# Optimization experiments

Hardware: AMD Instinct MI355X
Metric: run time of the kernel (lower is better)

Reference implementation:

```python
import jax, jax.numpy as jnp
import numpy as np

# dims: S samples, J u-functions, D outputs, P input dims, N data points
S, J, D, P, N = 8, 4, 4, 3, 1024
BG, BU, MG, MU = 32, 32, 10, 32  # g-RFF, u-RFF, g-inducing, u-inducing


def setup_inputs() -> dict:
    key = jax.random.key(0)
    ks = jax.random.split(key, 16)
    ts = jax.random.normal(ks[0], (N, P), dtype=jnp.float32)
    alphas = jax.random.uniform(ks[1], (D, P), minval=0.5, maxval=1.5)   # filter window precisions
    pgs = jax.random.uniform(ks[2], (D, P), minval=0.5, maxval=1.5)      # g kernel precisions (ls2pr)
    zgs = jnp.tile(jnp.linspace(-1.0, 1.0, MG, dtype=jnp.float32)[:, None], (1, P))  # g inducing inputs
    thetag = 2.0 * jax.random.normal(ks[3], (D, P, BG))                  # g spectral freqs
    betag = jax.random.uniform(ks[4], (S, D, P, BG), minval=0.0, maxval=2 * np.pi)
    wg = jax.random.normal(ks[5], (S, D, P, BG)) / np.sqrt(BG)           # g RFF weights
    qg = 0.1 * jax.random.normal(ks[6], (S, D, P, MG))                   # g canonical weights (compute_q)
    pus = jax.random.uniform(ks[7], (P,), minval=0.5, maxval=1.5)        # u cross-kernel precisions
    zus = jax.random.normal(ks[8], (MU, P))                              # u inducing inputs
    thetau = 2.0 * jax.random.normal(ks[9], (S, J, P, BU))               # u spectral freqs
    betau = jax.random.uniform(ks[10], (S, J, BU), minval=0.0, maxval=2 * np.pi)
    wu = jax.random.normal(ks[11], (S, J, BU)) / np.sqrt(BU)
    qu = 0.1 * jax.random.normal(ks[12], (S, J, MU))                     # u canonical weights
    ampu = jnp.float32(1.0)
    log_amps = 0.1 * jax.random.normal(ks[13], (D, J))
    W = jax.random.normal(ks[14], (P, D)) / np.sqrt(P)
    return dict(ts=ts, alphas=alphas, pgs=pgs, zgs=zgs, thetag=thetag, betag=betag,
                wg=wg, qg=qg, pus=pus, zus=zus, thetau=thetau, betau=betau,
                wu=wu, qu=qu, ampu=ampu, log_amps=log_amps, W=W)


def reference(ts, alphas, pgs, zgs, thetag, betag, wg, qg, pus, zus,
              thetau, betau, wu, qu, ampu, log_amps, W):
    """NPGPLayer.forward: f_d(t) = sum_j amps[d,j] * I_dj(t) + ts @ W, where
    I_dj(t) = ampu * int_{R^P} [prod_p exp(-alpha_dp tau_p^2) g_dp(tau_p)] u_j(t - tau) dtau,
    with g, u sampled via random-Fourier + canonical (inducing) features; all 1-D
    Gaussian x cosine integrals are closed-form (this is the math of integrals.full_I)."""
    pi = jnp.pi
    amps = jnp.exp(log_amps)  # [D,J]

    # ---------- Part A: u RFF terms.  Fourier transform of windowed g at om ----------
    om = thetau  # [S,J,P,BU]
    aE = alphas[None, None, :, :, None, None]            # [1,1,D,P,1,1]
    th = thetag[None, None, :, :, None, :]               # [1,1,D,P,1,BG]
    omE = om[:, :, None, :, :, None]                     # [S,J,1,P,BU,1]
    e1 = jnp.exp(-(th - omE) ** 2 / (4 * aE))
    e2 = jnp.exp(-(th + omE) ** 2 / (4 * aE))
    cb = jnp.cos(betag)[:, None, :, :, None, :]
    sb = jnp.sin(betag)[:, None, :, :, None, :]
    wgE = wg[:, None, :, :, None, :]
    # int exp(-a tau^2) cos(th tau + b) e^{-i om tau} dtau
    Ghat_rff = jnp.sum(0.5 * jnp.sqrt(pi / aE) * wgE * ((e1 + e2) * cb + 1j * (e1 - e2) * sb), axis=-1)  # [S,J,D,P,BU]

    A = alphas + pgs                                     # [D,P]
    zT = zgs.T                                           # [P,MG]
    mu = pgs[:, :, None] * zT[None] / A[:, :, None]      # [D,P,MG]
    rg = alphas[:, :, None] * pgs[:, :, None] * zT[None] ** 2 / A[:, :, None]
    decay = jnp.exp(-om[:, :, None, :, :] ** 2 / (4 * A[None, None, :, :, None]))        # [S,J,D,P,BU]
    phase_mu = jnp.exp(-1j * om[:, :, None, :, :, None] * mu[None, None, :, :, None, :])  # [S,J,D,P,BU,MG]
    can_coef = jnp.sqrt(pi / A)[..., None] * jnp.exp(-rg)                                 # [D,P,MG]
    Ghat_can = jnp.sum(qg[:, None, :, :, None, :] * can_coef[None, None, :, :, None, :] * phase_mu, axis=-1) * decay
    Ghat = Ghat_rff + Ghat_can                           # [S,J,D,P,BU] complex

    phase_t = jnp.exp(1j * om[..., None] * ts.T[None, None, :, None, :])  # [S,J,P,BU,N]
    combined = Ghat[..., None] * phase_t[:, :, None]     # [S,J,D,P,BU,N]
    prodp = jnp.prod(combined, axis=3)                   # [S,J,D,BU,N]  (product over input dims)
    cu = wu * jnp.exp(1j * betau)                        # [S,J,BU]
    F_rff = jnp.real(jnp.einsum('sjb,sjdbn->sjdn', cu, prodp))

    # ---------- Part B: u canonical (inducing) terms -- Gaussian x Gaussian integrals ----------
    c = jnp.transpose(ts[:, None, :] - zus[None, :, :], (2, 0, 1))  # [P,N,MU]
    Bm = alphas + pus[None, :]                           # [D,P]
    mp = pus[None, :, None, None] * c[None] / Bm[:, :, None, None]                 # [D,P,N,MU]
    rp = alphas[:, :, None, None] * pus[None, :, None, None] * c[None] ** 2 / Bm[:, :, None, None]
    spec = jnp.sqrt(pi / Bm)[:, :, None] * jnp.exp(-thetag ** 2 / (4 * Bm[:, :, None]))  # [D,P,BG]
    arg = thetag[:, :, None, None, :] * mp[..., None]    # [D,P,N,MU,BG]
    cosx, sinx = jnp.cos(arg), jnp.sin(arg)
    coef1 = wg * jnp.cos(betag) * spec[None]             # [S,D,P,BG]
    coef2 = wg * jnp.sin(betag) * spec[None]
    term_rff = (jnp.einsum('dpnmb,sdpb->sdpnm', cosx, coef1)
                - jnp.einsum('dpnmb,sdpb->sdpnm', sinx, coef2)) * jnp.exp(-rp)[None]
    Cm = Bm + pgs                                        # [D,P]
    diff = mp[..., None] - zT[None, :, None, None, :]    # [D,P,N,MU,MG]
    r2 = Bm[:, :, None, None, None] * pgs[:, :, None, None, None] * diff ** 2 / Cm[:, :, None, None, None]
    val = jnp.sqrt(pi / Cm)[:, :, None, None, None] * jnp.exp(-rp[..., None] - r2)
    term_can = jnp.einsum('dpnmg,sdpg->sdpnm', val, qg)
    Gg = term_rff + term_can                             # [S,D,P,N,MU]
    prodg = jnp.prod(Gg, axis=2)                         # [S,D,N,MU]
    F_can = jnp.einsum('sjm,sdnm->sjdn', qu, prodg)

    F = ampu * (F_rff + F_can)                           # [S,J,D,N]
    layer = jnp.einsum('dj,sjdn->snd', amps, F)          # amps-weighted sum over u functions
    return layer + ts @ W                                # residual connection (is_final_layer=False)
```

## Files before the change

kernel.cpp:

```cpp
#include <hip/hip_runtime.h>
#include <math.h>

#define S_ 8
#define J_ 4
#define D_ 4
#define P_ 3
#define N_ 1024
#define BG_ 32
#define BU_ 32
#define MG_ 10
#define MU_ 32

static constexpr float PI_F = 3.14159265358979323846f;

#define COEF_OFF    0
#define CANPART_OFF 8192

#define NB_COEF 64
#define NB_CAN  512

__global__ __launch_bounds__(256, 4) void fused_kernel(
    const float* __restrict__ ts,     const float* __restrict__ alphas,
    const float* __restrict__ pgs,    const float* __restrict__ zgs,
    const float* __restrict__ thetag, const float* __restrict__ betag,
    const float* __restrict__ wg,     const float* __restrict__ qg,
    const float* __restrict__ pus,    const float* __restrict__ zus,
    const float* __restrict__ thetau, const float* __restrict__ betau,
    const float* __restrict__ wu,     const float* __restrict__ qu,
    const float* __restrict__ ampu_p, const float* __restrict__ log_amps,
    float* __restrict__ ws)
{
    int bid = blockIdx.x;
    int t   = threadIdx.x;
    float ampu = ampu_p[0];

    if (bid >= NB_COEF) {
        __shared__ float sc1[P_][BG_][S_];
        __shared__ float sc2[P_][BG_][S_];
        __shared__ float sqg[P_][MG_][S_];
        __shared__ float stg[P_][BG_];
        __shared__ float szg[P_][MG_];
        __shared__ float szu[P_][MU_];
        __shared__ float sts[8][P_];
        __shared__ float squ[S_][MU_];
        __shared__ float skmp[P_], skrp[P_], sksc[P_], skbc[P_];

        int cb = bid - NB_COEF;
        int d  = cb >> 7;
        int n0 = (cb & 127) * 8;

        for (int i = t; i < P_*BG_*S_; i += 256) {
            int p = i >> 8, b = (i >> 3) & 31, s = i & 7;
            float alpha = alphas[d*P_ + p];
            float Bm = alpha + pus[p];
            float th = thetag[(d*P_ + p)*BG_ + b];
            float spec = sqrtf(PI_F / Bm) * __expf(-th*th*0.25f/Bm);
            float be = betag[((s*D_ + d)*P_ + p)*BG_ + b];
            float w  = wg   [((s*D_ + d)*P_ + p)*BG_ + b];
            float sb, cbv; __sincosf(be, &sb, &cbv);
            sc1[p][b][s] = w * cbv * spec;
            sc2[p][b][s] = w * sb * spec;
        }
        for (int i = t; i < P_*MG_*S_; i += 256) {
            int p = i / (MG_*S_), r = i % (MG_*S_), g = r >> 3, s = r & 7;
            ((float*)sqg)[i] = qg[((s*D_ + d)*P_ + p)*MG_ + g];
        }
        {
            int s = t >> 5, m = t & 31;
            float acc = 0.f;
            #pragma unroll
            for (int j = 0; j < J_; ++j)
                acc += __expf(log_amps[d*J_ + j]) * qu[(s*J_ + j)*MU_ + m];
            squ[s][m] = ampu * acc;
        }
        if (t < P_*BG_) ((float*)stg)[t] = thetag[d*P_*BG_ + t];
        if (t < P_*MG_) { int p = t / MG_, g = t % MG_; szg[p][g] = zgs[g*P_ + p]; }
        if (t >= 128 && t < 128 + P_*MU_) {
            int i = t - 128; int p = i >> 5, m = i & 31;
            szu[p][m] = zus[m*P_ + p];
        }
        if (t >= 96 && t < 96 + 8*P_) { int i = t - 96; sts[i/3][i%3] = ts[n0*P_ + i]; }
        if (t >= 120 && t < 120 + P_) {
            int p = t - 120;
            float alpha = alphas[d*P_ + p], pg = pgs[d*P_ + p], pu = pus[p];
            float Bm = alpha + pu, invB = 1.f / Bm;
            skmp[p] = pu * invB;
            skrp[p] = alpha * pu * invB;
            float Cm = Bm + pg, invC = 1.f / Cm;
            sksc[p] = sqrtf(PI_F * invC);
            skbc[p] = Bm * pg * invC;
        }
        __syncthreads();

        int m = t & 31, q = (t >> 5) & 1, nl = t >> 6;
        int rA = nl*2, rB = nl*2 + 1;

        float pA0=1.f,pA1=1.f,pA2=1.f,pA3=1.f,pA4=1.f,pA5=1.f,pA6=1.f,pA7=1.f;
        float pB0=1.f,pB1=1.f,pB2=1.f,pB3=1.f,pB4=1.f,pB5=1.f,pB6=1.f,pB7=1.f;

        #pragma unroll 1
        for (int p = 0; p < P_; ++p) {
            float zu = szu[p][m];
            float cA = sts[rA][p] - zu;
            float cB = sts[rB][p] - zu;
            float mpA = skmp[p] * cA, mpB = skmp[p] * cB;
            float EA = __expf(-skrp[p] * cA * cA);
            float EB = __expf(-skrp[p] * cB * cB);

            float aA0=0.f,aA1=0.f,aA2=0.f,aA3=0.f,aA4=0.f,aA5=0.f,aA6=0.f,aA7=0.f;
            float aB0=0.f,aB1=0.f,aB2=0.f,aB3=0.f,aB4=0.f,aB5=0.f,aB6=0.f,aB7=0.f;

            int b0 = q * 16;
            #pragma unroll 2
            for (int bb = 0; bb < 16; ++bb) {
                int b = b0 + bb;
                float th = stg[p][b];
                float sxA, cxA; __sincosf(th * mpA, &sxA, &cxA);
                float sxB, cxB; __sincosf(th * mpB, &sxB, &cxB);
                const float4* c1v = (const float4*)&sc1[p][b][0];
                const float4* c2v = (const float4*)&sc2[p][b][0];
                float4 u0 = c1v[0], u1 = c1v[1];
                float4 v0 = c2v[0], v1 = c2v[1];
                aA0 += u0.x*cxA - v0.x*sxA;  aA1 += u0.y*cxA - v0.y*sxA;
                aA2 += u0.z*cxA - v0.z*sxA;  aA3 += u0.w*cxA - v0.w*sxA;
                aA4 += u1.x*cxA - v1.x*sxA;  aA5 += u1.y*cxA - v1.y*sxA;
                aA6 += u1.z*cxA - v1.z*sxA;  aA7 += u1.w*cxA - v1.w*sxA;
                aB0 += u0.x*cxB - v0.x*sxB;  aB1 += u0.y*cxB - v0.y*sxB;
                aB2 += u0.z*cxB - v0.z*sxB;  aB3 += u0.w*cxB - v0.w*sxB;
                aB4 += u1.x*cxB - v1.x*sxB;  aB5 += u1.y*cxB - v1.y*sxB;
                aB6 += u1.z*cxB - v1.z*sxB;  aB7 += u1.w*cxB - v1.w*sxB;
            }
            int g0 = q * 5;
            #pragma unroll 1
            for (int gg = 0; gg < 5; ++gg) {
                int g = g0 + gg;
                float zg = szg[p][g];
                float dA = mpA - zg, dB = mpB - zg;
                float vA = sksc[p] * __expf(-skbc[p]*dA*dA);
                float vB = sksc[p] * __expf(-skbc[p]*dB*dB);
                const float4* qv = (const float4*)&sqg[p][g][0];
                float4 q0 = qv[0], q1 = qv[1];
                aA0 += q0.x*vA; aA1 += q0.y*vA; aA2 += q0.z*vA; aA3 += q0.w*vA;
                aA4 += q1.x*vA; aA5 += q1.y*vA; aA6 += q1.z*vA; aA7 += q1.w*vA;
                aB0 += q0.x*vB; aB1 += q0.y*vB; aB2 += q0.z*vB; aB3 += q0.w*vB;
                aB4 += q1.x*vB; aB5 += q1.y*vB; aB6 += q1.z*vB; aB7 += q1.w*vB;
            }
            aA0 += __shfl_xor(aA0, 32, 64); aA1 += __shfl_xor(aA1, 32, 64);
            aA2 += __shfl_xor(aA2, 32, 64); aA3 += __shfl_xor(aA3, 32, 64);
            aA4 += __shfl_xor(aA4, 32, 64); aA5 += __shfl_xor(aA5, 32, 64);
            aA6 += __shfl_xor(aA6, 32, 64); aA7 += __shfl_xor(aA7, 32, 64);
            aB0 += __shfl_xor(aB0, 32, 64); aB1 += __shfl_xor(aB1, 32, 64);
            aB2 += __shfl_xor(aB2, 32, 64); aB3 += __shfl_xor(aB3, 32, 64);
            aB4 += __shfl_xor(aB4, 32, 64); aB5 += __shfl_xor(aB5, 32, 64);
            aB6 += __shfl_xor(aB6, 32, 64); aB7 += __shfl_xor(aB7, 32, 64);
            pA0 *= EA*aA0; pA1 *= EA*aA1; pA2 *= EA*aA2; pA3 *= EA*aA3;
            pA4 *= EA*aA4; pA5 *= EA*aA5; pA6 *= EA*aA6; pA7 *= EA*aA7;
            pB0 *= EB*aB0; pB1 *= EB*aB1; pB2 *= EB*aB2; pB3 *= EB*aB3;
            pB4 *= EB*aB4; pB5 *= EB*aB5; pB6 *= EB*aB6; pB7 *= EB*aB7;
        }

        float prodA[S_] = {pA0,pA1,pA2,pA3,pA4,pA5,pA6,pA7};
        float prodB[S_] = {pB0,pB1,pB2,pB3,pB4,pB5,pB6,pB7};
        int nA = n0 + rA, nB = n0 + rB;
        int s0 = q * 4;
        #pragma unroll
        for (int ss = 0; ss < 4; ++ss) {
            int s = ss + s0;
            float qu_sm = squ[s][m];
            float vA = qu_sm * prodA[s];
            float vB = qu_sm * prodB[s];
            #pragma unroll
            for (int off = 16; off; off >>= 1) {
                vA += __shfl_xor(vA, off, 32);
                vB += __shfl_xor(vB, off, 32);
            }
            if (m == 0) {
                ws[CANPART_OFF + (s*N_ + nA)*D_ + d] = vA;
                ws[CANPART_OFF + (s*N_ + nB)*D_ + d] = vB;
            }
        }
    } else {
        int gtid = bid * 256 + t;
        int q  = gtid & 3;
        int bu = (gtid >> 2) & 31;
        int d  = (gtid >> 7) & 3;
        int j  = (gtid >> 9) & 3;
        int s  = gtid >> 11;
        float G3r = 1.f, G3i = 0.f;
        #pragma unroll 1
        for (int p = 0; p < P_; ++p) {
            float alpha = alphas[d*P_ + p], pg = pgs[d*P_ + p];
            float om    = thetau[((s*J_ + j)*P_ + p)*BU_ + bu];
            float inv4a = 0.25f / alpha;
            float pref  = 0.5f * sqrtf(PI_F / alpha);
            float gr = 0.f, gi = 0.f;
            int b0 = q * 8;
            #pragma unroll 2
            for (int bb = 0; bb < 8; ++bb) {
                int b = b0 + bb;
                float th = thetag[(d*P_ + p)*BG_ + b];
                float dm = th - om, dpl = th + om;
                float e1 = __expf(-dm*dm*inv4a);
                float e2 = __expf(-dpl*dpl*inv4a);
                float be = betag[((s*D_ + d)*P_ + p)*BG_ + b];
                float w  = wg   [((s*D_ + d)*P_ + p)*BG_ + b];
                float sb, cb; __sincosf(be, &sb, &cb);
                gr += pref * w * (e1 + e2) * cb;
                gi += pref * w * (e1 - e2) * sb;
            }
            float A = alpha + pg, invA = 1.f / A;
            float decay = __expf(-om*om*0.25f*invA);
            float cc    = sqrtf(PI_F * invA);
            float cr = 0.f, ci = 0.f;
            int g0 = q * 3, gn = (q < 3) ? 3 : 1;
            #pragma unroll 1
            for (int gg = 0; gg < gn; ++gg) {
                int g = g0 + gg;
                float z  = zgs[g*P_ + p];
                float mu = pg * z * invA;
                float rg = alpha * pg * z * z * invA;
                float cg = cc * __expf(-rg);
                float qv = qg[((s*D_ + d)*P_ + p)*MG_ + g];
                float sm, cm; __sincosf(om * mu, &sm, &cm);
                cr += qv * cg * cm;
                ci -= qv * cg * sm;
            }
            #pragma unroll
            for (int off = 1; off < 4; off <<= 1) {
                gr += __shfl_xor(gr, off, 4);
                gi += __shfl_xor(gi, off, 4);
                cr += __shfl_xor(cr, off, 4);
                ci += __shfl_xor(ci, off, 4);
            }
            float Gr = gr + decay * cr;
            float Gi = gi + decay * ci;
            float nr = G3r*Gr - G3i*Gi;
            float ni = G3r*Gi + G3i*Gr;
            G3r = nr; G3i = ni;
        }
        if (q == 0) {
            float bv = betau[(s*J_ + j)*BU_ + bu];
            float wv = wu   [(s*J_ + j)*BU_ + bu];
            float sbu, cbu; __sincosf(bv, &sbu, &cbu);
            float cuR = wv * cbu, cuI = wv * sbu;
            float amp = ampu * __expf(log_amps[d*J_ + j]);
            int base = (((s*J_ + j)*BU_ + bu)*D_ + d) * 2;
            ws[COEF_OFF + base    ] = amp * (cuR*G3r - cuI*G3i);
            ws[COEF_OFF + base + 1] = amp * (cuR*G3i + cuI*G3r);
        }
    }
}

__global__ __launch_bounds__(256, 4) void final_kernel(
    const float* __restrict__ ts, const float* __restrict__ thetau,
    const float* __restrict__ W,  const float* __restrict__ ws,
    float* __restrict__ out)
{
    __shared__ float sth[J_][P_][BU_];
    __shared__ float scf[J_*BU_][8];
    __shared__ float sW[P_][D_];

    int bid = blockIdx.x;
    int s  = bid >> 7;
    int n0 = (bid & 127) * 8;
    int t  = threadIdx.x;

    for (int i = t; i < J_*P_*BU_; i += 256) ((float*)sth)[i] = thetau[s*J_*P_*BU_ + i];
    for (int i = t; i < J_*BU_*8; i += 256)  ((float*)scf)[i] = ws[COEF_OFF + s*J_*BU_*8 + i];
    if (t < P_*D_) ((float*)sW)[t] = W[t];
    __syncthreads();

    int k = t & 31, nl = t >> 5;
    int n = n0 + nl;
    float t0 = ts[n*P_], t1 = ts[n*P_ + 1], t2 = ts[n*P_ + 2];

    float r0=0.f, r1=0.f, r2=0.f, r3=0.f;
    #pragma unroll 2
    for (int j = 0; j < J_; ++j) {
        float phi = sth[j][0][k]*t0 + sth[j][1][k]*t1 + sth[j][2][k]*t2;
        float sp, cp; __sincosf(phi, &sp, &cp);
        const float4* cfv = (const float4*)&scf[j*BU_ + k][0];
        float4 u = cfv[0], v = cfv[1];
        r0 += u.x*cp - u.y*sp;
        r1 += u.z*cp - u.w*sp;
        r2 += v.x*cp - v.y*sp;
        r3 += v.z*cp - v.w*sp;
    }
    #pragma unroll
    for (int off = 16; off; off >>= 1) {
        r0 += __shfl_xor(r0, off, 32);
        r1 += __shfl_xor(r1, off, 32);
        r2 += __shfl_xor(r2, off, 32);
        r3 += __shfl_xor(r3, off, 32);
    }
    if (k == 0) {
        const float4 cpart = *(const float4*)(ws + CANPART_OFF + (s*N_ + n)*D_);
        float4 o;
        o.x = cpart.x + r0 + t0*sW[0][0] + t1*sW[1][0] + t2*sW[2][0];
        o.y = cpart.y + r1 + t0*sW[0][1] + t1*sW[1][1] + t2*sW[2][1];
        o.z = cpart.z + r2 + t0*sW[0][2] + t1*sW[1][2] + t2*sW[2][2];
        o.w = cpart.w + r3 + t0*sW[0][3] + t1*sW[1][3] + t2*sW[2][3];
        *(float4*)(out + (s*N_ + n)*D_) = o;
    }
}

extern "C" void kernel_launch(void* const* d_in, const int* in_sizes, int n_in,
                              void* d_out, int out_size, void* d_ws, size_t ws_size,
                              hipStream_t stream)
{
    const float* ts       = (const float*)d_in[0];
    const float* alphas   = (const float*)d_in[1];
    const float* pgs      = (const float*)d_in[2];
    const float* zgs      = (const float*)d_in[3];
    const float* thetag   = (const float*)d_in[4];
    const float* betag    = (const float*)d_in[5];
    const float* wg       = (const float*)d_in[6];
    const float* qg       = (const float*)d_in[7];
    const float* pus      = (const float*)d_in[8];
    const float* zus      = (const float*)d_in[9];
    const float* thetau   = (const float*)d_in[10];
    const float* betau    = (const float*)d_in[11];
    const float* wu       = (const float*)d_in[12];
    const float* qu       = (const float*)d_in[13];
    const float* ampu     = (const float*)d_in[14];
    const float* log_amps = (const float*)d_in[15];
    const float* W        = (const float*)d_in[16];
    float* ws  = (float*)d_ws;
    float* out = (float*)d_out;

    fused_kernel<<<NB_COEF + NB_CAN, 256, 0, stream>>>(
        ts, alphas, pgs, zgs, thetag, betag, wg, qg,
        pus, zus, thetau, betau, wu, qu, ampu, log_amps, ws);
    final_kernel<<<1024, 256, 0, stream>>>(ts, thetau, W, ws, out);
}
```

Measured before the change: 26.04 us.

## Fold coefficient computation into every canonical block with per-warp coefficient slices

```diff
diff --git a/kernel.cpp b/kernel.cpp
--- a/kernel.cpp
+++ b/kernel.cpp
@@ -16,7 +16,6 @@
 #define COEF_OFF    0
 #define CANPART_OFF 8192
 
-#define NB_COEF 64
 #define NB_CAN  512
 
 __global__ __launch_bounds__(256, 4) void fused_kernel(
@@ -30,223 +29,214 @@
     const float* __restrict__ ampu_p, const float* __restrict__ log_amps,
     float* __restrict__ ws)
 {
+    __shared__ float sc1[P_][BG_][S_];
+    __shared__ float sc2[P_][BG_][S_];
+    __shared__ float sqg[P_][MG_][S_];
+    __shared__ float stg[P_][BG_];
+    __shared__ float szg[P_][MG_];
+    __shared__ float szu[P_][MU_];
+    __shared__ float sts[8][P_];
+    __shared__ float squ[S_][MU_];
+    __shared__ float skmp[P_], skrp[P_], sksc[P_], skbc[P_];
+
     int bid = blockIdx.x;
     int t   = threadIdx.x;
     float ampu = ampu_p[0];
 
-    if (bid >= NB_COEF) {
-        __shared__ float sc1[P_][BG_][S_];
-        __shared__ float sc2[P_][BG_][S_];
-        __shared__ float sqg[P_][MG_][S_];
-        __shared__ float stg[P_][BG_];
-        __shared__ float szg[P_][MG_];
-        __shared__ float szu[P_][MU_];
-        __shared__ float sts[8][P_];
-        __shared__ float squ[S_][MU_];
-        __shared__ float skmp[P_], skrp[P_], sksc[P_], skbc[P_];
-
-        int cb = bid - NB_COEF;
-        int d  = cb >> 7;
-        int n0 = (cb & 127) * 8;
-
-        for (int i = t; i < P_*BG_*S_; i += 256) {
-            int p = i >> 8, b = (i >> 3) & 31, s = i & 7;
-            float alpha = alphas[d*P_ + p];
-            float Bm = alpha + pus[p];
-            float th = thetag[(d*P_ + p)*BG_ + b];
-            float spec = sqrtf(PI_F / Bm) * __expf(-th*th*0.25f/Bm);
-            float be = betag[((s*D_ + d)*P_ + p)*BG_ + b];
-            float w  = wg   [((s*D_ + d)*P_ + p)*BG_ + b];
-            float sb, cbv; __sincosf(be, &sb, &cbv);
-            sc1[p][b][s] = w * cbv * spec;
-            sc2[p][b][s] = w * sb * spec;
-        }
-        for (int i = t; i < P_*MG_*S_; i += 256) {
-            int p = i / (MG_*S_), r = i % (MG_*S_), g = r >> 3, s = r & 7;
-            ((float*)sqg)[i] = qg[((s*D_ + d)*P_ + p)*MG_ + g];
-        }
-        {
-            int s = t >> 5, m = t & 31;
-            float acc = 0.f;
-            #pragma unroll
-            for (int j = 0; j < J_; ++j)
-                acc += __expf(log_amps[d*J_ + j]) * qu[(s*J_ + j)*MU_ + m];
-            squ[s][m] = ampu * acc;
-        }
-        if (t < P_*BG_) ((float*)stg)[t] = thetag[d*P_*BG_ + t];
-        if (t < P_*MG_) { int p = t / MG_, g = t % MG_; szg[p][g] = zgs[g*P_ + p]; }
-        if (t >= 128 && t < 128 + P_*MU_) {
-            int i = t - 128; int p = i >> 5, m = i & 31;
-            szu[p][m] = zus[m*P_ + p];
-        }
-        if (t >= 96 && t < 96 + 8*P_) { int i = t - 96; sts[i/3][i%3] = ts[n0*P_ + i]; }
-        if (t >= 120 && t < 120 + P_) {
-            int p = t - 120;
-            float alpha = alphas[d*P_ + p], pg = pgs[d*P_ + p], pu = pus[p];
-            float Bm = alpha + pu, invB = 1.f / Bm;
-            skmp[p] = pu * invB;
-            skrp[p] = alpha * pu * invB;
-            float Cm = Bm + pg, invC = 1.f / Cm;
-            sksc[p] = sqrtf(PI_F * invC);
-            skbc[p] = Bm * pg * invC;
-        }
-        __syncthreads();
-
-        int m = t & 31, q = (t >> 5) & 1, nl = t >> 6;
-        int rA = nl*2, rB = nl*2 + 1;
-
-        float pA0=1.f,pA1=1.f,pA2=1.f,pA3=1.f,pA4=1.f,pA5=1.f,pA6=1.f,pA7=1.f;
-        float pB0=1.f,pB1=1.f,pB2=1.f,pB3=1.f,pB4=1.f,pB5=1.f,pB6=1.f,pB7=1.f;
-
-        #pragma unroll 1
-        for (int p = 0; p < P_; ++p) {
-            float zu = szu[p][m];
-            float cA = sts[rA][p] - zu;
-            float cB = sts[rB][p] - zu;
-            float mpA = skmp[p] * cA, mpB = skmp[p] * cB;
-            float EA = __expf(-skrp[p] * cA * cA);
-            float EB = __expf(-skrp[p] * cB * cB);
-
-            float aA0=0.f,aA1=0.f,aA2=0.f,aA3=0.f,aA4=0.f,aA5=0.f,aA6=0.f,aA7=0.f;
-            float aB0=0.f,aB1=0.f,aB2=0.f,aB3=0.f,aB4=0.f,aB5=0.f,aB6=0.f,aB7=0.f;
-
-            int b0 = q * 16;
-            #pragma unroll 2
-            for (int bb = 0; bb < 16; ++bb) {
-                int b = b0 + bb;
-                float th = stg[p][b];
-                float sxA, cxA; __sincosf(th * mpA, &sxA, &cxA);
-                float sxB, cxB; __sincosf(th * mpB, &sxB, &cxB);
-                const float4* c1v = (const float4*)&sc1[p][b][0];
-                const float4* c2v = (const float4*)&sc2[p][b][0];
-                float4 u0 = c1v[0], u1 = c1v[1];
-                float4 v0 = c2v[0], v1 = c2v[1];
-                aA0 += u0.x*cxA - v0.x*sxA;  aA1 += u0.y*cxA - v0.y*sxA;
-                aA2 += u0.z*cxA - v0.z*sxA;  aA3 += u0.w*cxA - v0.w*sxA;
-                aA4 += u1.x*cxA - v1.x*sxA;  aA5 += u1.y*cxA - v1.y*sxA;
-                aA6 += u1.z*cxA - v1.z*sxA;  aA7 += u1.w*cxA - v1.w*sxA;
-                aB0 += u0.x*cxB - v0.x*sxB;  aB1 += u0.y*cxB - v0.y*sxB;
-                aB2 += u0.z*cxB - v0.z*sxB;  aB3 += u0.w*cxB - v0.w*sxB;
-                aB4 += u1.x*cxB - v1.x*sxB;  aB5 += u1.y*cxB - v1.y*sxB;
-                aB6 += u1.z*cxB - v1.z*sxB;  aB7 += u1.w*cxB - v1.w*sxB;
-            }
-            int g0 = q * 5;
-            #pragma unroll 1
-            for (int gg = 0; gg < 5; ++gg) {
-                int g = g0 + gg;
-                float zg = szg[p][g];
-                float dA = mpA - zg, dB = mpB - zg;
-                float vA = sksc[p] * __expf(-skbc[p]*dA*dA);
-                float vB = sksc[p] * __expf(-skbc[p]*dB*dB);
-                const float4* qv = (const float4*)&sqg[p][g][0];
-                float4 q0 = qv[0], q1 = qv[1];
-                aA0 += q0.x*vA; aA1 += q0.y*vA; aA2 += q0.z*vA; aA3 += q0.w*vA;
-                aA4 += q1.x*vA; aA5 += q1.y*vA; aA6 += q1.z*vA; aA7 += q1.w*vA;
-                aB0 += q0.x*vB; aB1 += q0.y*vB; aB2 += q0.z*vB; aB3 += q0.w*vB;
-                aB4 += q1.x*vB; aB5 += q1.y*vB; aB6 += q1.z*vB; aB7 += q1.w*vB;
-            }
-            aA0 += __shfl_xor(aA0, 32, 64); aA1 += __shfl_xor(aA1, 32, 64);
-            aA2 += __shfl_xor(aA2, 32, 64); aA3 += __shfl_xor(aA3, 32, 64);
-            aA4 += __shfl_xor(aA4, 32, 64); aA5 += __shfl_xor(aA5, 32, 64);
-            aA6 += __shfl_xor(aA6, 32, 64); aA7 += __shfl_xor(aA7, 32, 64);
-            aB0 += __shfl_xor(aB0, 32, 64); aB1 += __shfl_xor(aB1, 32, 64);
-            aB2 += __shfl_xor(aB2, 32, 64); aB3 += __shfl_xor(aB3, 32, 64);
-            aB4 += __shfl_xor(aB4, 32, 64); aB5 += __shfl_xor(aB5, 32, 64);
-            aB6 += __shfl_xor(aB6, 32, 64); aB7 += __shfl_xor(aB7, 32, 64);
-            pA0 *= EA*aA0; pA1 *= EA*aA1; pA2 *= EA*aA2; pA3 *= EA*aA3;
-            pA4 *= EA*aA4; pA5 *= EA*aA5; pA6 *= EA*aA6; pA7 *= EA*aA7;
-            pB0 *= EB*aB0; pB1 *= EB*aB1; pB2 *= EB*aB2; pB3 *= EB*aB3;
-            pB4 *= EB*aB4; pB5 *= EB*aB5; pB6 *= EB*aB6; pB7 *= EB*aB7;
-        }
-
-        float prodA[S_] = {pA0,pA1,pA2,pA3,pA4,pA5,pA6,pA7};
-        float prodB[S_] = {pB0,pB1,pB2,pB3,pB4,pB5,pB6,pB7};
-        int nA = n0 + rA, nB = n0 + rB;
-        int s0 = q * 4;
-        #pragma unroll
-        for (int ss = 0; ss < 4; ++ss) {
-            int s = ss + s0;
-            float qu_sm = squ[s][m];
-            float vA = qu_sm * prodA[s];
-            float vB = qu_sm * prodB[s];
-            #pragma unroll
-            for (int off = 16; off; off >>= 1) {
-                vA += __shfl_xor(vA, off, 32);
-                vB += __shfl_xor(vB, off, 32);
-            }
-            if (m == 0) {
-                ws[CANPART_OFF + (s*N_ + nA)*D_ + d] = vA;
-                ws[CANPART_OFF + (s*N_ + nB)*D_ + d] = vB;
-            }
-        }
-    } else {
-        int gtid = bid * 256 + t;
-        int q  = gtid & 3;
-        int bu = (gtid >> 2) & 31;
-        int d  = (gtid >> 7) & 3;
-        int j  = (gtid >> 9) & 3;
-        int s  = gtid >> 11;
+    int d  = bid >> 7;
+    int n0 = (bid & 127) * 8;
+
+    {
+        int l  = t & 31;
+        int vl = t >> 5;
+        int v  = bid * 8 + vl;
+        int bu = v & 31, dc = (v >> 5) & 3, j = (v >> 7) & 3, s = v >> 9;
+
         float G3r = 1.f, G3i = 0.f;
         #pragma unroll 1
         for (int p = 0; p < P_; ++p) {
-            float alpha = alphas[d*P_ + p], pg = pgs[d*P_ + p];
+            float alpha = alphas[dc*P_ + p], pg = pgs[dc*P_ + p];
             float om    = thetau[((s*J_ + j)*P_ + p)*BU_ + bu];
+            float A = alpha + pg, invA = 1.f / A;
+
             float inv4a = 0.25f / alpha;
             float pref  = 0.5f * sqrtf(PI_F / alpha);
-            float gr = 0.f, gi = 0.f;
-            int b0 = q * 8;
-            #pragma unroll 2
-            for (int bb = 0; bb < 8; ++bb) {
-                int b = b0 + bb;
-                float th = thetag[(d*P_ + p)*BG_ + b];
-                float dm = th - om, dpl = th + om;
-                float e1 = __expf(-dm*dm*inv4a);
-                float e2 = __expf(-dpl*dpl*inv4a);
-                float be = betag[((s*D_ + d)*P_ + p)*BG_ + b];
-                float w  = wg   [((s*D_ + d)*P_ + p)*BG_ + b];
-                float sb, cb; __sincosf(be, &sb, &cb);
-                gr += pref * w * (e1 + e2) * cb;
-                gi += pref * w * (e1 - e2) * sb;
-            }
-            float A = alpha + pg, invA = 1.f / A;
-            float decay = __expf(-om*om*0.25f*invA);
-            float cc    = sqrtf(PI_F * invA);
+            float th = thetag[(dc*P_ + p)*BG_ + l];
+            float dm = th - om, dpl = th + om;
+            float e1 = __expf(-dm*dm*inv4a);
+            float e2 = __expf(-dpl*dpl*inv4a);
+            float be = betag[((s*D_ + dc)*P_ + p)*BG_ + l];
+            float w  = wg   [((s*D_ + dc)*P_ + p)*BG_ + l];
+            float sb, cb; __sincosf(be, &sb, &cb);
+            float gr = pref * w * (e1 + e2) * cb;
+            float gi = pref * w * (e1 - e2) * sb;
+
             float cr = 0.f, ci = 0.f;
-            int g0 = q * 3, gn = (q < 3) ? 3 : 1;
-            #pragma unroll 1
-            for (int gg = 0; gg < gn; ++gg) {
-                int g = g0 + gg;
-                float z  = zgs[g*P_ + p];
+            if (l < MG_) {
+                float cc = sqrtf(PI_F * invA);
+                float z  = zgs[l*P_ + p];
                 float mu = pg * z * invA;
                 float rg = alpha * pg * z * z * invA;
                 float cg = cc * __expf(-rg);
-                float qv = qg[((s*D_ + d)*P_ + p)*MG_ + g];
+                float qv = qg[((s*D_ + dc)*P_ + p)*MG_ + l];
                 float sm, cm; __sincosf(om * mu, &sm, &cm);
-                cr += qv * cg * cm;
-                ci -= qv * cg * sm;
+                cr =  qv * cg * cm;
+                ci = -qv * cg * sm;
             }
             #pragma unroll
-            for (int off = 1; off < 4; off <<= 1) {
-                gr += __shfl_xor(gr, off, 4);
-                gi += __shfl_xor(gi, off, 4);
-                cr += __shfl_xor(cr, off, 4);
-                ci += __shfl_xor(ci, off, 4);
+            for (int off = 16; off; off >>= 1) {
+                gr += __shfl_xor(gr, off, 32);
+                gi += __shfl_xor(gi, off, 32);
+                cr += __shfl_xor(cr, off, 32);
+                ci += __shfl_xor(ci, off, 32);
             }
+            float decay = __expf(-om*om*0.25f*invA);
             float Gr = gr + decay * cr;
             float Gi = gi + decay * ci;
             float nr = G3r*Gr - G3i*Gi;
             float ni = G3r*Gi + G3i*Gr;
             G3r = nr; G3i = ni;
         }
-        if (q == 0) {
+        if (l == 0) {
             float bv = betau[(s*J_ + j)*BU_ + bu];
             float wv = wu   [(s*J_ + j)*BU_ + bu];
             float sbu, cbu; __sincosf(bv, &sbu, &cbu);
             float cuR = wv * cbu, cuI = wv * sbu;
-            float amp = ampu * __expf(log_amps[d*J_ + j]);
-            int base = (((s*J_ + j)*BU_ + bu)*D_ + d) * 2;
+            float amp = ampu * __expf(log_amps[dc*J_ + j]);
+            int base = (((s*J_ + j)*BU_ + bu)*D_ + dc) * 2;
             ws[COEF_OFF + base    ] = amp * (cuR*G3r - cuI*G3i);
             ws[COEF_OFF + base + 1] = amp * (cuR*G3i + cuI*G3r);
+        }
+    }
+
+    for (int i = t; i < P_*BG_*S_; i += 256) {
+        int p = i >> 8, b = (i >> 3) & 31, s = i & 7;
+        float alpha = alphas[d*P_ + p];
+        float Bm = alpha + pus[p];
+        float th = thetag[(d*P_ + p)*BG_ + b];
+        float spec = sqrtf(PI_F / Bm) * __expf(-th*th*0.25f/Bm);
+        float be = betag[((s*D_ + d)*P_ + p)*BG_ + b];
+        float w  = wg   [((s*D_ + d)*P_ + p)*BG_ + b];
+        float sb, cbv; __sincosf(be, &sb, &cbv);
+        sc1[p][b][s] = w * cbv * spec;
+        sc2[p][b][s] = w * sb * spec;
+    }
+    for (int i = t; i < P_*MG_*S_; i += 256) {
+        int p = i / (MG_*S_), r = i % (MG_*S_), g = r >> 3, s = r & 7;
+        ((float*)sqg)[i] = qg[((s*D_ + d)*P_ + p)*MG_ + g];
+    }
+    {
+        int s = t >> 5, m = t & 31;
+        float acc = 0.f;
+        #pragma unroll
+        for (int j = 0; j < J_; ++j)
+            acc += __expf(log_amps[d*J_ + j]) * qu[(s*J_ + j)*MU_ + m];
+        squ[s][m] = ampu * acc;
+    }
+    if (t < P_*BG_) ((float*)stg)[t] = thetag[d*P_*BG_ + t];
+    if (t < P_*MG_) { int p = t / MG_, g = t % MG_; szg[p][g] = zgs[g*P_ + p]; }
+    if (t >= 128 && t < 128 + P_*MU_) {
+        int i = t - 128; int p = i >> 5, m = i & 31;
+        szu[p][m] = zus[m*P_ + p];
+    }
+    if (t >= 96 && t < 96 + 8*P_) { int i = t - 96; sts[i/3][i%3] = ts[n0*P_ + i]; }
+    if (t >= 120 && t < 120 + P_) {
+        int p = t - 120;
+        float alpha = alphas[d*P_ + p], pg = pgs[d*P_ + p], pu = pus[p];
+        float Bm = alpha + pu, invB = 1.f / Bm;
+        skmp[p] = pu * invB;
+        skrp[p] = alpha * pu * invB;
+        float Cm = Bm + pg, invC = 1.f / Cm;
+        sksc[p] = sqrtf(PI_F * invC);
+        skbc[p] = Bm * pg * invC;
+    }
+    __syncthreads();
+
+    int m = t & 31, q = (t >> 5) & 1, nl = t >> 6;
+    int rA = nl*2, rB = nl*2 + 1;
+
+    float pA0=1.f,pA1=1.f,pA2=1.f,pA3=1.f,pA4=1.f,pA5=1.f,pA6=1.f,pA7=1.f;
+    float pB0=1.f,pB1=1.f,pB2=1.f,pB3=1.f,pB4=1.f,pB5=1.f,pB6=1.f,pB7=1.f;
+
+    #pragma unroll 1
+    for (int p = 0; p < P_; ++p) {
+        float zu = szu[p][m];
+        float cA = sts[rA][p] - zu;
+        float cB = sts[rB][p] - zu;
+        float mpA = skmp[p] * cA, mpB = skmp[p] * cB;
+        float EA = __expf(-skrp[p] * cA * cA);
+        float EB = __expf(-skrp[p] * cB * cB);
+
+        float aA0=0.f,aA1=0.f,aA2=0.f,aA3=0.f,aA4=0.f,aA5=0.f,aA6=0.f,aA7=0.f;
+        float aB0=0.f,aB1=0.f,aB2=0.f,aB3=0.f,aB4=0.f,aB5=0.f,aB6=0.f,aB7=0.f;
+
+        int b0 = q * 16;
+        #pragma unroll 2
+        for (int bb = 0; bb < 16; ++bb) {
+            int b = b0 + bb;
+            float th = stg[p][b];
+            float sxA, cxA; __sincosf(th * mpA, &sxA, &cxA);
+            float sxB, cxB; __sincosf(th * mpB, &sxB, &cxB);
+            const float4* c1v = (const float4*)&sc1[p][b][0];
+            const float4* c2v = (const float4*)&sc2[p][b][0];
+            float4 u0 = c1v[0], u1 = c1v[1];
+            float4 v0 = c2v[0], v1 = c2v[1];
+            aA0 += u0.x*cxA - v0.x*sxA;  aA1 += u0.y*cxA - v0.y*sxA;
+            aA2 += u0.z*cxA - v0.z*sxA;  aA3 += u0.w*cxA - v0.w*sxA;
+            aA4 += u1.x*cxA - v1.x*sxA;  aA5 += u1.y*cxA - v1.y*sxA;
+            aA6 += u1.z*cxA - v1.z*sxA;  aA7 += u1.w*cxA - v1.w*sxA;
+            aB0 += u0.x*cxB - v0.x*sxB;  aB1 += u0.y*cxB - v0.y*sxB;
+            aB2 += u0.z*cxB - v0.z*sxB;  aB3 += u0.w*cxB - v0.w*sxB;
+            aB4 += u1.x*cxB - v1.x*sxB;  aB5 += u1.y*cxB - v1.y*sxB;
+            aB6 += u1.z*cxB - v1.z*sxB;  aB7 += u1.w*cxB - v1.w*sxB;
+        }
+        int g0 = q * 5;
+        #pragma unroll 1
+        for (int gg = 0; gg < 5; ++gg) {
+            int g = g0 + gg;
+            float zg = szg[p][g];
+            float dA = mpA - zg, dB = mpB - zg;
+            float vA = sksc[p] * __expf(-skbc[p]*dA*dA);
+            float vB = sksc[p] * __expf(-skbc[p]*dB*dB);
+            const float4* qv = (const float4*)&sqg[p][g][0];
+            float4 q0 = qv[0], q1 = qv[1];
+            aA0 += q0.x*vA; aA1 += q0.y*vA; aA2 += q0.z*vA; aA3 += q0.w*vA;
+            aA4 += q1.x*vA; aA5 += q1.y*vA; aA6 += q1.z*vA; aA7 += q1.w*vA;
+            aB0 += q0.x*vB; aB1 += q0.y*vB; aB2 += q0.z*vB; aB3 += q0.w*vB;
+            aB4 += q1.x*vB; aB5 += q1.y*vB; aB6 += q1.z*vB; aB7 += q1.w*vB;
+        }
+        aA0 += __shfl_xor(aA0, 32, 64); aA1 += __shfl_xor(aA1, 32, 64);
+        aA2 += __shfl_xor(aA2, 32, 64); aA3 += __shfl_xor(aA3, 32, 64);
+        aA4 += __shfl_xor(aA4, 32, 64); aA5 += __shfl_xor(aA5, 32, 64);
+        aA6 += __shfl_xor(aA6, 32, 64); aA7 += __shfl_xor(aA7, 32, 64);
+        aB0 += __shfl_xor(aB0, 32, 64); aB1 += __shfl_xor(aB1, 32, 64);
+        aB2 += __shfl_xor(aB2, 32, 64); aB3 += __shfl_xor(aB3, 32, 64);
+        aB4 += __shfl_xor(aB4, 32, 64); aB5 += __shfl_xor(aB5, 32, 64);
+        aB6 += __shfl_xor(aB6, 32, 64); aB7 += __shfl_xor(aB7, 32, 64);
+        pA0 *= EA*aA0; pA1 *= EA*aA1; pA2 *= EA*aA2; pA3 *= EA*aA3;
+        pA4 *= EA*aA4; pA5 *= EA*aA5; pA6 *= EA*aA6; pA7 *= EA*aA7;
+        pB0 *= EB*aB0; pB1 *= EB*aB1; pB2 *= EB*aB2; pB3 *= EB*aB3;
+        pB4 *= EB*aB4; pB5 *= EB*aB5; pB6 *= EB*aB6; pB7 *= EB*aB7;
+    }
+
+    float prodA[S_] = {pA0,pA1,pA2,pA3,pA4,pA5,pA6,pA7};
+    float prodB[S_] = {pB0,pB1,pB2,pB3,pB4,pB5,pB6,pB7};
+    int nA = n0 + rA, nB = n0 + rB;
+    int s0 = q * 4;
+    #pragma unroll
+    for (int ss = 0; ss < 4; ++ss) {
+        int s = ss + s0;
+        float qu_sm = squ[s][m];
+        float vA = qu_sm * prodA[s];
+        float vB = qu_sm * prodB[s];
+        #pragma unroll
+        for (int off = 16; off; off >>= 1) {
+            vA += __shfl_xor(vA, off, 32);
+            vB += __shfl_xor(vB, off, 32);
+        }
+        if (m == 0) {
+            ws[CANPART_OFF + (s*N_ + nA)*D_ + d] = vA;
+            ws[CANPART_OFF + (s*N_ + nB)*D_ + d] = vB;
         }
     }
 }
@@ -328,7 +318,7 @@
     float* ws  = (float*)d_ws;
     float* out = (float*)d_out;
 
-    fused_kernel<<<NB_COEF + NB_CAN, 256, 0, stream>>>(
+    fused_kernel<<<NB_CAN, 256, 0, stream>>>(
         ts, alphas, pgs, zgs, thetag, betag, wg, qg,
         pus, zus, thetau, betau, wu, qu, ampu, log_amps, ws);
     final_kernel<<<1024, 256, 0, stream>>>(ts, thetau, W, ws, out);
```

New measurement: 27.34 us. 1.05x slower.
